# Kernel tuning notes

Measured on AMD Instinct MI355X. Metric: run time of the kernel, lower is better.

Reference implementation:

```python
import jax, jax.numpy as jnp
import numpy as np

B, N, F, H = 32, 1024, 128, 128
NEG_BIG = -1e10


def setup_inputs() -> dict:
    key = jax.random.key(0)
    ks = jax.random.split(key, 8)
    M_features = jax.random.normal(ks[0], (B, N, F), dtype=jnp.float32)
    adj = (jax.random.uniform(ks[1], (B, N, N)) < 0.05).astype(jnp.float32)
    eye = jnp.eye(N, dtype=jnp.float32)[None]
    M_adjacency = jnp.maximum(adj, eye)
    mask = (jnp.arange(N)[None, :] < (3 * N) // 4).astype(jnp.float32)
    mask = jnp.broadcast_to(mask, (B, N)).astype(jnp.float32)
    he = lambda k, shp: jax.random.normal(k, shp, jnp.float32) * np.sqrt(2.0 / shp[0])
    W_layer = he(ks[2], (F, H))
    b_layer = jnp.zeros((H,), jnp.float32)
    W_att_self = he(ks[3], (H, 1))
    W_att_neighbor = he(ks[4], (H, 1))
    return {"M_features": M_features, "M_adjacency": M_adjacency, "mask": mask,
            "W_layer": W_layer, "b_layer": b_layer,
            "W_att_self": W_att_self, "W_att_neighbor": W_att_neighbor}


def reference(M_features, M_adjacency, mask, W_layer, b_layer, W_att_self, W_att_neighbor):
    # hidden features: [B, N, H]
    h = jnp.einsum('bnf,fh->bnh', M_features, W_layer)
    # additive attention logits: self score + neighbor score (broadcast) -> [B, N, N]
    a_self = jnp.einsum('bnh,ho->bno', h, W_att_self)          # [B, N, 1]
    a_neigh = jnp.einsum('bnh,ho->bno', h, W_att_neighbor)     # [B, N, 1]
    logits = a_self + jnp.transpose(a_neigh, (0, 2, 1))        # [B, N, N]
    logits = jax.nn.leaky_relu(logits, negative_slope=0.2)     # tf default alpha=0.2
    logits = logits + NEG_BIG * (1.0 - M_adjacency)
    attention = jax.nn.softmax(logits, axis=-1)
    # eval mode: no dropout
    h_prime = jnp.einsum('bnm,bmh->bnh', attention, h) + b_layer[None, None, :]
    h_prime = h_prime * mask[:, :, None]
    return h_prime


if __name__ == '__main__':
    out = reference(**setup_inputs())
    print(out.shape, out.dtype)
```

## Files before the change

### kernel.cpp

```cpp
#include <hip/hip_runtime.h>
#include <math.h>

#define BATCH 32
#define NN 1024
#define FF 128
#define HH 128
#define NODES 32

typedef __attribute__((ext_vector_type(8))) short short8v;
typedef __attribute__((ext_vector_type(4))) float f32x4;

__device__ __forceinline__ unsigned short f2bf(float f) {
    unsigned u = __float_as_uint(f);
    u += 0x7fffu + ((u >> 16) & 1u);
    return (unsigned short)(u >> 16);
}

__global__ __launch_bounds__(128) void gat_hidden(
    const float* __restrict__ X,
    const float* __restrict__ W,
    const float* __restrict__ Wself,
    const float* __restrict__ Wneigh,
    unsigned short* __restrict__ g,
    float* __restrict__ a_self,
    float* __restrict__ a_neigh)
{
    __shared__ float xs[NODES][FF];
    __shared__ float hs[NODES][HH + 1];
    const int tid = threadIdx.x;
    const long base_node = (long)blockIdx.x * NODES;
    const int batch = (int)(base_node >> 10);
    const int kc = (int)((base_node & 1023) >> 5);

    const float4* X4 = (const float4*)(X + base_node * FF);
    float4* xs4 = (float4*)&xs[0][0];
#pragma unroll
    for (int k = 0; k < (NODES * FF) / (4 * 128); k++)
        xs4[k * 128 + tid] = X4[k * 128 + tid];
    __syncthreads();

    float acc[NODES];
#pragma unroll
    for (int n = 0; n < NODES; n++) acc[n] = 0.f;
    const int c = tid;
    for (int fq = 0; fq < FF / 4; fq++) {
        const float w0 = W[(4 * fq + 0) * HH + c];
        const float w1 = W[(4 * fq + 1) * HH + c];
        const float w2 = W[(4 * fq + 2) * HH + c];
        const float w3 = W[(4 * fq + 3) * HH + c];
#pragma unroll
        for (int n = 0; n < NODES; n++) {
            const float4 x4 = *(const float4*)&xs[n][4 * fq];
            acc[n] += x4.x * w0 + x4.y * w1 + x4.z * w2 + x4.w * w3;
        }
    }
    {
        const int ct = c >> 4, li = c & 15;
        unsigned short* gb = g + ((((size_t)batch * 32 + kc) * 8 + ct) * 64) * 8;
        union { uint4 q; unsigned short u[8]; } pk;
#pragma unroll
        for (int kg = 0; kg < 4; kg++) {
#pragma unroll
            for (int e = 0; e < 8; e++) pk.u[e] = f2bf(acc[kg * 8 + e]);
            *(uint4*)(gb + (kg * 16 + li) * 8) = pk.q;
        }
    }
#pragma unroll
    for (int n = 0; n < NODES; n++) hs[n][c] = acc[n];
    __syncthreads();

    if (tid < 2 * NODES) {
        const int n = tid & (NODES - 1);
        const float* wvp = (tid < NODES) ? Wself : Wneigh;
        float s = 0.f;
        for (int cc = 0; cc < HH; cc++) s += hs[n][cc] * wvp[cc];
        if (tid < NODES) a_self[base_node + n] = s;
        else             a_neigh[base_node + n] = s;
    }
}

#define PROW 72
__global__ __launch_bounds__(256) void gat_attend(
    const float* __restrict__ adj,
    const float* __restrict__ mask,
    const unsigned short* __restrict__ g,
    const float* __restrict__ a_self,
    const float* __restrict__ a_neigh,
    float* __restrict__ part0, float* __restrict__ part1,
    float* __restrict__ rs0, float* __restrict__ rs1)
{
    const int tid = threadIdx.x;
    const int lane = tid & 63;
    const int wv = tid >> 6;
    const int b = blockIdx.x;
    const int xcd = b & 7;
    const int rest = b >> 3;
    const int batch = xcd * 4 + (rest >> 5);
    const int idx = rest & 31;
    const int tile = idx >> 1;
    const int chunk = idx & 1;
    const int r0 = batch * NN + tile * 64;

    if (mask[r0] == 0.f) return;

    __shared__ unsigned short P[2][64 * PROW];
    __shared__ float rsums[64][16];

    const int k0c = chunk * 512;
    const int srow = tid >> 4;
    const int scf4 = tid & 15;
    const float4* arow[4];
    float aslv[4];
#pragma unroll
    for (int i = 0; i < 4; i++) {
        const int rr = i * 16 + srow;
        arow[i] = (const float4*)(adj + (size_t)(r0 + rr) * NN + k0c);
        aslv[i] = a_self[r0 + rr];
    }
    const float4* anp = (const float4*)(a_neigh + batch * NN + k0c);
    const unsigned short* gb = g + (size_t)batch * 131072;

    float rsp[4] = {0.f, 0.f, 0.f, 0.f};

#define STAGE(t, buf)                                                      \
    {                                                                      \
        const float4 an4 = anp[(t) * 16 + scf4];                           \
        const float4 a0 = arow[0][(t) * 16 + scf4];                        \
        const float4 a1 = arow[1][(t) * 16 + scf4];                        \
        const float4 a2 = arow[2][(t) * 16 + scf4];                        \
        const float4 a3 = arow[3][(t) * 16 + scf4];                        \
        union { unsigned short u[4]; uint2 q; } w0, w1, w2, w3;            \
        float x, p;                                                        \
        x = aslv[0] + an4.x; p = (a0.x > 0.f) ? __expf(fmaxf(x, 0.2f * x)) : 0.f; w0.u[0] = f2bf(p); rsp[0] += __uint_as_float((unsigned)w0.u[0] << 16); \
        x = aslv[0] + an4.y; p = (a0.y > 0.f) ? __expf(fmaxf(x, 0.2f * x)) : 0.f; w0.u[1] = f2bf(p); rsp[0] += __uint_as_float((unsigned)w0.u[1] << 16); \
        x = aslv[0] + an4.z; p = (a0.z > 0.f) ? __expf(fmaxf(x, 0.2f * x)) : 0.f; w0.u[2] = f2bf(p); rsp[0] += __uint_as_float((unsigned)w0.u[2] << 16); \
        x = aslv[0] + an4.w; p = (a0.w > 0.f) ? __expf(fmaxf(x, 0.2f * x)) : 0.f; w0.u[3] = f2bf(p); rsp[0] += __uint_as_float((unsigned)w0.u[3] << 16); \
        x = aslv[1] + an4.x; p = (a1.x > 0.f) ? __expf(fmaxf(x, 0.2f * x)) : 0.f; w1.u[0] = f2bf(p); rsp[1] += __uint_as_float((unsigned)w1.u[0] << 16); \
        x = aslv[1] + an4.y; p = (a1.y > 0.f) ? __expf(fmaxf(x, 0.2f * x)) : 0.f; w1.u[1] = f2bf(p); rsp[1] += __uint_as_float((unsigned)w1.u[1] << 16); \
        x = aslv[1] + an4.z; p = (a1.z > 0.f) ? __expf(fmaxf(x, 0.2f * x)) : 0.f; w1.u[2] = f2bf(p); rsp[1] += __uint_as_float((unsigned)w1.u[2] << 16); \
        x = aslv[1] + an4.w; p = (a1.w > 0.f) ? __expf(fmaxf(x, 0.2f * x)) : 0.f; w1.u[3] = f2bf(p); rsp[1] += __uint_as_float((unsigned)w1.u[3] << 16); \
        x = aslv[2] + an4.x; p = (a2.x > 0.f) ? __expf(fmaxf(x, 0.2f * x)) : 0.f; w2.u[0] = f2bf(p); rsp[2] += __uint_as_float((unsigned)w2.u[0] << 16); \
        x = aslv[2] + an4.y; p = (a2.y > 0.f) ? __expf(fmaxf(x, 0.2f * x)) : 0.f; w2.u[1] = f2bf(p); rsp[2] += __uint_as_float((unsigned)w2.u[1] << 16); \
        x = aslv[2] + an4.z; p = (a2.z > 0.f) ? __expf(fmaxf(x, 0.2f * x)) : 0.f; w2.u[2] = f2bf(p); rsp[2] += __uint_as_float((unsigned)w2.u[2] << 16); \
        x = aslv[2] + an4.w; p = (a2.w > 0.f) ? __expf(fmaxf(x, 0.2f * x)) : 0.f; w2.u[3] = f2bf(p); rsp[2] += __uint_as_float((unsigned)w2.u[3] << 16); \
        x = aslv[3] + an4.x; p = (a3.x > 0.f) ? __expf(fmaxf(x, 0.2f * x)) : 0.f; w3.u[0] = f2bf(p); rsp[3] += __uint_as_float((unsigned)w3.u[0] << 16); \
        x = aslv[3] + an4.y; p = (a3.y > 0.f) ? __expf(fmaxf(x, 0.2f * x)) : 0.f; w3.u[1] = f2bf(p); rsp[3] += __uint_as_float((unsigned)w3.u[1] << 16); \
        x = aslv[3] + an4.z; p = (a3.z > 0.f) ? __expf(fmaxf(x, 0.2f * x)) : 0.f; w3.u[2] = f2bf(p); rsp[3] += __uint_as_float((unsigned)w3.u[2] << 16); \
        x = aslv[3] + an4.w; p = (a3.w > 0.f) ? __expf(fmaxf(x, 0.2f * x)) : 0.f; w3.u[3] = f2bf(p); rsp[3] += __uint_as_float((unsigned)w3.u[3] << 16); \
        *(uint2*)&P[buf][(0 * 16 + srow) * PROW + scf4 * 4] = w0.q;        \
        *(uint2*)&P[buf][(1 * 16 + srow) * PROW + scf4 * 4] = w1.q;        \
        *(uint2*)&P[buf][(2 * 16 + srow) * PROW + scf4 * 4] = w2.q;        \
        *(uint2*)&P[buf][(3 * 16 + srow) * PROW + scf4 * 4] = w3.q;        \
    }

    f32x4 acc[8];
#pragma unroll
    for (int ct = 0; ct < 8; ct++)
#pragma unroll
        for (int i = 0; i < 4; i++) acc[ct][i] = 0.f;

    STAGE(0, 0)
    __syncthreads();

    const int li = lane & 15;
    const int kg8 = (lane >> 4) * 8;
    for (int it = 0; it < 8; ++it) {
        const int cur = it & 1;
#pragma unroll
        for (int kcl = 0; kcl < 2; kcl++) {
            const short8v af = *(const short8v*)&P[cur][(wv * 16 + li) * PROW + kcl * 32 + kg8];
            const int kcG = (k0c >> 5) + it * 2 + kcl;
#pragma unroll
            for (int ct = 0; ct < 8; ct++) {
                const short8v bf = *(const short8v*)(gb + ((size_t)(kcG * 8 + ct) * 64 + lane) * 8);
                acc[ct] = __builtin_amdgcn_mfma_f32_16x16x32_bf16(af, bf, acc[ct], 0, 0, 0);
            }
        }
        if (it < 7) STAGE(it + 1, cur ^ 1)
        __syncthreads();
    }

    rsums[0 * 16 + srow][scf4] = rsp[0];
    rsums[1 * 16 + srow][scf4] = rsp[1];
    rsums[2 * 16 + srow][scf4] = rsp[2];
    rsums[3 * 16 + srow][scf4] = rsp[3];
    __syncthreads();
    float* rsP = chunk ? rs1 : rs0;
    if (tid < 64) {
        float s = 0.f;
#pragma unroll
        for (int q = 0; q < 16; q++) s += rsums[tid][q];
        rsP[r0 + tid] = s;
    }

    float* pP = chunk ? part1 : part0;
#pragma unroll
    for (int ct = 0; ct < 8; ct++)
#pragma unroll
        for (int i = 0; i < 4; i++) {
            const int r = wv * 16 + (lane >> 4) * 4 + i;
            pP[(size_t)(r0 + r) * HH + ct * 16 + li] = acc[ct][i];
        }
#undef STAGE
}

__global__ __launch_bounds__(256) void gat_combine(
    const float* __restrict__ mask,
    const float* __restrict__ part0, const float* __restrict__ part1,
    const float* __restrict__ rs0, const float* __restrict__ rs1,
    const float* __restrict__ bvec,
    float* __restrict__ out)
{
    const int t = threadIdx.x;
    const int row = blockIdx.x * 8 + (t >> 5);
    const int c4 = (t & 31) * 4;
    const size_t o = (size_t)row * HH + c4;

    if (mask[row] == 0.f) {
        *(float4*)(out + o) = make_float4(0.f, 0.f, 0.f, 0.f);
        return;
    }
    const float4 a = *(const float4*)(part0 + o);
    const float4 b = *(const float4*)(part1 + o);
    const float inv = 1.f / (rs0[row] + rs1[row]);
    const float4 bv = *(const float4*)(bvec + c4);
    float4 r;
    r.x = (a.x + b.x) * inv + bv.x;
    r.y = (a.y + b.y) * inv + bv.y;
    r.z = (a.z + b.z) * inv + bv.z;
    r.w = (a.w + b.w) * inv + bv.w;
    *(float4*)(out + o) = r;
}

extern "C" void kernel_launch(void* const* d_in, const int* in_sizes, int n_in,
                              void* d_out, int out_size, void* d_ws, size_t ws_size,
                              hipStream_t stream) {
    const float* X      = (const float*)d_in[0];
    const float* adj    = (const float*)d_in[1];
    const float* mask   = (const float*)d_in[2];
    const float* W      = (const float*)d_in[3];
    const float* bvec   = (const float*)d_in[4];
    const float* Wself  = (const float*)d_in[5];
    const float* Wneigh = (const float*)d_in[6];
    float* out = (float*)d_out;

    char* wsb = (char*)d_ws;
    unsigned short* g = (unsigned short*)wsb;
    const size_t GSZ = (size_t)BATCH * NN * HH * 2;
    float* a_self  = (float*)(wsb + GSZ);
    float* a_neigh = a_self + (size_t)BATCH * NN;
    float* rs0     = a_neigh + (size_t)BATCH * NN;
    float* rs1     = rs0 + (size_t)BATCH * NN;
    float* part0   = rs1 + (size_t)BATCH * NN;
    float* part1   = part0 + (size_t)BATCH * NN * HH;

    gat_hidden<<<(BATCH * NN) / NODES, 128, 0, stream>>>(
        X, W, Wself, Wneigh, g, a_self, a_neigh);
    gat_attend<<<1024, 256, 0, stream>>>(
        adj, mask, g, a_self, a_neigh, part0, part1, rs0, rs1);
    gat_combine<<<(BATCH * NN) / 8, 256, 0, stream>>>(
        mask, part0, part1, rs0, rs1, bvec, out);
}
```

Baseline: 70.08 us.

## Halve attend row tile to 32 and split columns across waves; XCD-map combine

The attend kernel now processes 32 rows per block instead of 64. Its four waves split as two row halves by two column halves, each holding 4 accumulators instead of 8, and the grid doubles to 2048 blocks. This raises occupancy and parallelism and cuts register pressure. In exchange each block reads g twice as often relative to its rows. The combine kernel also remaps block indices so each XCD handles the same batches as in attend, which targets L2 locality for the partial results.

Result: no change. 70.06 us (-0.0%).

```diff
diff --git a/kernel.cpp b/kernel.cpp
--- a/kernel.cpp
+++ b/kernel.cpp
@@ -6,6 +6,7 @@
 #define FF 128
 #define HH 128
 #define NODES 32
+#define PROW 72
 
 typedef __attribute__((ext_vector_type(8))) short short8v;
 typedef __attribute__((ext_vector_type(4))) float f32x4;
@@ -79,7 +80,6 @@
     }
 }
 
-#define PROW 72
 __global__ __launch_bounds__(256) void gat_attend(
     const float* __restrict__ adj,
     const float* __restrict__ mask,
@@ -95,67 +95,56 @@
     const int b = blockIdx.x;
     const int xcd = b & 7;
     const int rest = b >> 3;
-    const int batch = xcd * 4 + (rest >> 5);
-    const int idx = rest & 31;
+    const int batch = xcd * 4 + (rest >> 6);
+    const int idx = rest & 63;
     const int tile = idx >> 1;
     const int chunk = idx & 1;
-    const int r0 = batch * NN + tile * 64;
+    const int r0 = batch * NN + tile * 32;
 
     if (mask[r0] == 0.f) return;
 
-    __shared__ unsigned short P[2][64 * PROW];
-    __shared__ float rsums[64][16];
+    __shared__ unsigned short P[2][32 * PROW];
+    __shared__ float rsums[32][16];
 
     const int k0c = chunk * 512;
     const int srow = tid >> 4;
     const int scf4 = tid & 15;
-    const float4* arow[4];
-    float aslv[4];
-#pragma unroll
-    for (int i = 0; i < 4; i++) {
-        const int rr = i * 16 + srow;
-        arow[i] = (const float4*)(adj + (size_t)(r0 + rr) * NN + k0c);
-        aslv[i] = a_self[r0 + rr];
-    }
+    const float4* ar0 = (const float4*)(adj + (size_t)(r0 + srow) * NN + k0c);
+    const float4* ar1 = (const float4*)(adj + (size_t)(r0 + srow + 16) * NN + k0c);
     const float4* anp = (const float4*)(a_neigh + batch * NN + k0c);
+    const float asl0 = a_self[r0 + srow];
+    const float asl1 = a_self[r0 + srow + 16];
     const unsigned short* gb = g + (size_t)batch * 131072;
 
-    float rsp[4] = {0.f, 0.f, 0.f, 0.f};
-
-#define STAGE(t, buf)                                                      \
-    {                                                                      \
-        const float4 an4 = anp[(t) * 16 + scf4];                           \
-        const float4 a0 = arow[0][(t) * 16 + scf4];                        \
-        const float4 a1 = arow[1][(t) * 16 + scf4];                        \
-        const float4 a2 = arow[2][(t) * 16 + scf4];                        \
-        const float4 a3 = arow[3][(t) * 16 + scf4];                        \
-        union { unsigned short u[4]; uint2 q; } w0, w1, w2, w3;            \
-        float x, p;                                                        \
-        x = aslv[0] + an4.x; p = (a0.x > 0.f) ? __expf(fmaxf(x, 0.2f * x)) : 0.f; w0.u[0] = f2bf(p); rsp[0] += __uint_as_float((unsigned)w0.u[0] << 16); \
-        x = aslv[0] + an4.y; p = (a0.y > 0.f) ? __expf(fmaxf(x, 0.2f * x)) : 0.f; w0.u[1] = f2bf(p); rsp[0] += __uint_as_float((unsigned)w0.u[1] << 16); \
-        x = aslv[0] + an4.z; p = (a0.z > 0.f) ? __expf(fmaxf(x, 0.2f * x)) : 0.f; w0.u[2] = f2bf(p); rsp[0] += __uint_as_float((unsigned)w0.u[2] << 16); \
-        x = aslv[0] + an4.w; p = (a0.w > 0.f) ? __expf(fmaxf(x, 0.2f * x)) : 0.f; w0.u[3] = f2bf(p); rsp[0] += __uint_as_float((unsigned)w0.u[3] << 16); \
-        x = aslv[1] + an4.x; p = (a1.x > 0.f) ? __expf(fmaxf(x, 0.2f * x)) : 0.f; w1.u[0] = f2bf(p); rsp[1] += __uint_as_float((unsigned)w1.u[0] << 16); \
-        x = aslv[1] + an4.y; p = (a1.y > 0.f) ? __expf(fmaxf(x, 0.2f * x)) : 0.f; w1.u[1] = f2bf(p); rsp[1] += __uint_as_float((unsigned)w1.u[1] << 16); \
-        x = aslv[1] + an4.z; p = (a1.z > 0.f) ? __expf(fmaxf(x, 0.2f * x)) : 0.f; w1.u[2] = f2bf(p); rsp[1] += __uint_as_float((unsigned)w1.u[2] << 16); \
-        x = aslv[1] + an4.w; p = (a1.w > 0.f) ? __expf(fmaxf(x, 0.2f * x)) : 0.f; w1.u[3] = f2bf(p); rsp[1] += __uint_as_float((unsigned)w1.u[3] << 16); \
-        x = aslv[2] + an4.x; p = (a2.x > 0.f) ? __expf(fmaxf(x, 0.2f * x)) : 0.f; w2.u[0] = f2bf(p); rsp[2] += __uint_as_float((unsigned)w2.u[0] << 16); \
-        x = aslv[2] + an4.y; p = (a2.y > 0.f) ? __expf(fmaxf(x, 0.2f * x)) : 0.f; w2.u[1] = f2bf(p); rsp[2] += __uint_as_float((unsigned)w2.u[1] << 16); \
-        x = aslv[2] + an4.z; p = (a2.z > 0.f) ? __expf(fmaxf(x, 0.2f * x)) : 0.f; w2.u[2] = f2bf(p); rsp[2] += __uint_as_float((unsigned)w2.u[2] << 16); \
-        x = aslv[2] + an4.w; p = (a2.w > 0.f) ? __expf(fmaxf(x, 0.2f * x)) : 0.f; w2.u[3] = f2bf(p); rsp[2] += __uint_as_float((unsigned)w2.u[3] << 16); \
-        x = aslv[3] + an4.x; p = (a3.x > 0.f) ? __expf(fmaxf(x, 0.2f * x)) : 0.f; w3.u[0] = f2bf(p); rsp[3] += __uint_as_float((unsigned)w3.u[0] << 16); \
-        x = aslv[3] + an4.y; p = (a3.y > 0.f) ? __expf(fmaxf(x, 0.2f * x)) : 0.f; w3.u[1] = f2bf(p); rsp[3] += __uint_as_float((unsigned)w3.u[1] << 16); \
-        x = aslv[3] + an4.z; p = (a3.z > 0.f) ? __expf(fmaxf(x, 0.2f * x)) : 0.f; w3.u[2] = f2bf(p); rsp[3] += __uint_as_float((unsigned)w3.u[2] << 16); \
-        x = aslv[3] + an4.w; p = (a3.w > 0.f) ? __expf(fmaxf(x, 0.2f * x)) : 0.f; w3.u[3] = f2bf(p); rsp[3] += __uint_as_float((unsigned)w3.u[3] << 16); \
-        *(uint2*)&P[buf][(0 * 16 + srow) * PROW + scf4 * 4] = w0.q;        \
-        *(uint2*)&P[buf][(1 * 16 + srow) * PROW + scf4 * 4] = w1.q;        \
-        *(uint2*)&P[buf][(2 * 16 + srow) * PROW + scf4 * 4] = w2.q;        \
-        *(uint2*)&P[buf][(3 * 16 + srow) * PROW + scf4 * 4] = w3.q;        \
-    }
-
-    f32x4 acc[8];
-#pragma unroll
-    for (int ct = 0; ct < 8; ct++)
+    float rsr0 = 0.f, rsr1 = 0.f;
+
+#define EW(a4, n4, aslv, rsv, rr, buf)                                               \
+    {                                                                                \
+        union { unsigned short u[4]; uint2 q; } wq;                                  \
+        float x, p;                                                                  \
+        x = aslv + n4.x; p = (a4.x > 0.f) ? __expf(fmaxf(x, 0.2f * x)) : 0.f;        \
+        wq.u[0] = f2bf(p); rsv += __uint_as_float((unsigned)wq.u[0] << 16);          \
+        x = aslv + n4.y; p = (a4.y > 0.f) ? __expf(fmaxf(x, 0.2f * x)) : 0.f;        \
+        wq.u[1] = f2bf(p); rsv += __uint_as_float((unsigned)wq.u[1] << 16);          \
+        x = aslv + n4.z; p = (a4.z > 0.f) ? __expf(fmaxf(x, 0.2f * x)) : 0.f;        \
+        wq.u[2] = f2bf(p); rsv += __uint_as_float((unsigned)wq.u[2] << 16);          \
+        x = aslv + n4.w; p = (a4.w > 0.f) ? __expf(fmaxf(x, 0.2f * x)) : 0.f;        \
+        wq.u[3] = f2bf(p); rsv += __uint_as_float((unsigned)wq.u[3] << 16);          \
+        *(uint2*)&P[buf][(rr) * PROW + scf4 * 4] = wq.q;                             \
+    }
+#define STAGE(t, buf)                                 \
+    {                                                 \
+        const int o = (t) * 16 + scf4;                \
+        const float4 an4 = anp[o];                    \
+        const float4 a0 = ar0[o];                     \
+        const float4 a1 = ar1[o];                     \
+        EW(a0, an4, asl0, rsr0, srow, buf)            \
+        EW(a1, an4, asl1, rsr1, srow + 16, buf)       \
+    }
+
+    f32x4 acc[4];
+#pragma unroll
+    for (int ct = 0; ct < 4; ct++)
 #pragma unroll
         for (int i = 0; i < 4; i++) acc[ct][i] = 0.f;
 
@@ -164,29 +153,30 @@
 
     const int li = lane & 15;
     const int kg8 = (lane >> 4) * 8;
+    const int rbase = (wv & 1) * 16;
+    const int cg = (wv >> 1) * 4;
+
     for (int it = 0; it < 8; ++it) {
         const int cur = it & 1;
 #pragma unroll
         for (int kcl = 0; kcl < 2; kcl++) {
-            const short8v af = *(const short8v*)&P[cur][(wv * 16 + li) * PROW + kcl * 32 + kg8];
-            const int kcG = (k0c >> 5) + it * 2 + kcl;
-#pragma unroll
-            for (int ct = 0; ct < 8; ct++) {
-                const short8v bf = *(const short8v*)(gb + ((size_t)(kcG * 8 + ct) * 64 + lane) * 8);
-                acc[ct] = __builtin_amdgcn_mfma_f32_16x16x32_bf16(af, bf, acc[ct], 0, 0, 0);
+            const short8v af = *(const short8v*)&P[cur][(rbase + li) * PROW + kcl * 32 + kg8];
+            const int kcG = chunk * 16 + it * 2 + kcl;
+#pragma unroll
+            for (int ctl = 0; ctl < 4; ctl++) {
+                const short8v bf = *(const short8v*)(gb + ((size_t)(kcG * 8 + cg + ctl) * 64 + lane) * 8);
+                acc[ctl] = __builtin_amdgcn_mfma_f32_16x16x32_bf16(af, bf, acc[ctl], 0, 0, 0);
             }
         }
         if (it < 7) STAGE(it + 1, cur ^ 1)
         __syncthreads();
     }
 
-    rsums[0 * 16 + srow][scf4] = rsp[0];
-    rsums[1 * 16 + srow][scf4] = rsp[1];
-    rsums[2 * 16 + srow][scf4] = rsp[2];
-    rsums[3 * 16 + srow][scf4] = rsp[3];
+    rsums[srow][scf4] = rsr0;
+    rsums[srow + 16][scf4] = rsr1;
     __syncthreads();
     float* rsP = chunk ? rs1 : rs0;
-    if (tid < 64) {
+    if (tid < 32) {
         float s = 0.f;
 #pragma unroll
         for (int q = 0; q < 16; q++) s += rsums[tid][q];
@@ -195,12 +185,13 @@
 
     float* pP = chunk ? part1 : part0;
 #pragma unroll
-    for (int ct = 0; ct < 8; ct++)
+    for (int ctl = 0; ctl < 4; ctl++)
 #pragma unroll
         for (int i = 0; i < 4; i++) {
-            const int r = wv * 16 + (lane >> 4) * 4 + i;
-            pP[(size_t)(r0 + r) * HH + ct * 16 + li] = acc[ct][i];
-        }
+            const int r = rbase + (lane >> 4) * 4 + i;
+            pP[(size_t)(r0 + r) * HH + (cg + ctl) * 16 + li] = acc[ctl][i];
+        }
+#undef EW
 #undef STAGE
 }
 
@@ -212,7 +203,12 @@
     float* __restrict__ out)
 {
     const int t = threadIdx.x;
-    const int row = blockIdx.x * 8 + (t >> 5);
+    const int b = blockIdx.x;
+    const int xcd = b & 7;
+    const int rest = b >> 3;
+    const int batch = xcd * 4 + (rest >> 7);
+    const int rowi = (rest & 127) * 8 + (t >> 5);
+    const int row = batch * NN + rowi;
     const int c4 = (t & 31) * 4;
     const size_t o = (size_t)row * HH + c4;
 
@@ -221,14 +217,14 @@
         return;
     }
     const float4 a = *(const float4*)(part0 + o);
-    const float4 b = *(const float4*)(part1 + o);
+    const float4 bq = *(const float4*)(part1 + o);
     const float inv = 1.f / (rs0[row] + rs1[row]);
     const float4 bv = *(const float4*)(bvec + c4);
     float4 r;
-    r.x = (a.x + b.x) * inv + bv.x;
-    r.y = (a.y + b.y) * inv + bv.y;
-    r.z = (a.z + b.z) * inv + bv.z;
-    r.w = (a.w + b.w) * inv + bv.w;
+    r.x = (a.x + bq.x) * inv + bv.x;
+    r.y = (a.y + bq.y) * inv + bv.y;
+    r.z = (a.z + bq.z) * inv + bv.z;
+    r.w = (a.w + bq.w) * inv + bv.w;
     *(float4*)(out + o) = r;
 }
 
@@ -256,8 +252,8 @@
 
     gat_hidden<<<(BATCH * NN) / NODES, 128, 0, stream>>>(
         X, W, Wself, Wneigh, g, a_self, a_neigh);
-    gat_attend<<<1024, 256, 0, stream>>>(
+    gat_attend<<<2048, 256, 0, stream>>>(
         adj, mask, g, a_self, a_neigh, part0, part1, rs0, rs1);
-    gat_combine<<<(BATCH * NN) / 8, 256, 0, stream>>>(
+    gat_combine<<<4096, 256, 0, stream>>>(
         mask, part0, part1, rs0, rs1, bvec, out);
 }
```
